# Kernel tuning notes

Hardware: AMD Instinct MI355X
Metric: run time of the kernel (lower is better)

Reference implementation:

```python
import jax, jax.numpy as jnp
import numpy as np

BS, SEQ, D_IN, D_OUT = 4, 1024, 1024, 1024
N_SKILLS, RANK = 8, 4
SCALING = 1.0  # lora_alpha / rank, folded into one constant
NEG_INF = -1e38


def setup_inputs() -> dict:
    key = jax.random.key(0)
    ks = jax.random.split(key, 5)
    x = jax.random.normal(ks[0], (BS, SEQ, D_IN), jnp.float32)
    phi = jax.random.normal(ks[1], (D_IN, N_SKILLS), jnp.float32) * 0.02
    lora_a = jax.random.normal(ks[2], (N_SKILLS, D_IN, RANK), jnp.float32) * 0.02
    lora_b = jax.random.normal(ks[3], (N_SKILLS, RANK, D_OUT), jnp.float32) * 0.02
    W = jax.random.normal(ks[4], (D_OUT, D_IN), jnp.float32) * 0.02
    b = jnp.zeros((D_OUT,), jnp.float32)
    # left-padded sequences with an instruction prefix right after the padding
    pad_len = np.array([100, 0, 250, 50])
    inst_len = 300
    pad = np.zeros((BS, SEQ), np.int32)
    inst = np.zeros((BS, SEQ), np.int32)
    for i in range(BS):
        pad[i, pad_len[i]:] = 1
        inst[i, pad_len[i]:pad_len[i] + inst_len] = 1
    return {"x": x, "phi": phi, "lora_a": lora_a, "lora_b": lora_b,
            "W": W, "b": b,
            "inst_mask": jnp.asarray(inst), "pad_mask": jnp.asarray(pad)}


def _causal_prefix_mask(inst_mask, pad_mask):
    # faithful port of create_causal_prefix_mask (padding_side='left')
    bs, seq = inst_mask.shape
    first_one = jnp.argmax(inst_mask, axis=1, keepdims=True)          # [b,1]
    n_ones = jnp.sum(inst_mask, axis=1, keepdims=True)                # [b,1]
    thresh = first_one + n_ones                                       # last_one_idx + 1
    exp = jnp.broadcast_to(thresh, (bs, seq))                         # [b,s]
    inv = jnp.maximum(seq - exp - jnp.arange(seq)[None, :], 0)[:, ::-1]
    m = (exp + inv) * pad_mask                                        # [b,s]
    m3 = m[:, :, None] * pad_mask[:, None, :]                         # [b,s,s]
    ar = jnp.arange(seq)[None, None, :]
    return ar < m3                                                    # bool [b,s,s]


def reference(x, phi, lora_a, lora_b, W, b, inst_mask, pad_mask):
    # router: mixing logits per token per skill
    mw = jnp.einsum('bsd,dn->bsn', x, phi)                            # [b,s,k]
    cm = _causal_prefix_mask(inst_mask, pad_mask)                     # [b,s,s]
    padf = pad_mask.astype(x.dtype)
    # expand over attended positions p, mask, softmax over p
    logits = jnp.where(cm[..., None], mw[:, :, None, :], NEG_INF)     # [b,s,p,k]
    logits = jnp.transpose(logits, (0, 3, 1, 2))                      # [b,k,s,p]
    D = jax.nn.softmax(logits, axis=-1)
    D = D * padf[:, None, :, None]                                    # zero padded query rows
    # token mixing: contract over source tokens (last axis of D)
    input_mixed = jnp.einsum('bsd,bkps->bkpd', x, D)                  # [b,k,s,d]
    # per-skill LoRA (n_splits == 1, q squeezed)
    ar_r = jnp.einsum('bksd,kdr->bskr', input_mixed, lora_a)          # [b,s,k,r]
    ad = jnp.einsum('bskr,krd->bskd', ar_r, lora_b)                   # [b,s,k,d_out]
    # softmax-weighted combine over skills
    C = jax.nn.softmax(mw, axis=-1)
    adapter_out = jnp.einsum('bsk,bskd->bsd', C, ad) * SCALING
    base = jnp.einsum('bsd,od->bso', x, W) + b
    return base + adapter_out
```

## Files before the change

### kernel.cpp

```cpp
#include <hip/hip_runtime.h>
#include <hip/hip_bf16.h>
#include <cstdint>

#define SEQ   1024
#define DOUT  1024
#define KDIM  1024
#define MTOT  4096

typedef __bf16 bf16x8 __attribute__((ext_vector_type(8)));
typedef float  f32x4  __attribute__((ext_vector_type(4)));
typedef unsigned short ushort8v __attribute__((ext_vector_type(8)));

__device__ inline unsigned short f2bf(float f) {
  union { float f; unsigned u; } a; a.f = f;
  unsigned r = a.u + 0x7fff + ((a.u >> 16) & 1);
  return (unsigned short)(r >> 16);
}

__device__ inline void gl16(const void* g, void* l) {
  __builtin_amdgcn_global_load_lds((__attribute__((address_space(1))) void*)g,
                                   (__attribute__((address_space(3))) void*)l, 16, 0, 0);
}

__device__ inline void barf() {
  asm volatile("" ::: "memory");
  __builtin_amdgcn_s_barrier();
  asm volatile("" ::: "memory");
}

__global__ __launch_bounds__(256) void k_prep(const float* __restrict__ phi, const float* __restrict__ la,
                                              const float* __restrict__ lb, const int* __restrict__ inst,
                                              unsigned short* __restrict__ Wc, unsigned short* __restrict__ B2T,
                                              int* __restrict__ thr) {
  int blk = blockIdx.x, tid = threadIdx.x;
  if (blk < 192) {
    int i = blk * 256 + tid;
    int row = 1024 + (i >> 10), d = i & 1023;
    float v;
    if (row < 1032)       v = phi[d * 8 + (row - 1024)];
    else if (row < 1064)  { int kr = row - 1032; v = la[(kr >> 2) * 4096 + d * 4 + (kr & 3)]; }
    else                  v = 0.f;
    Wc[(size_t)row * 1024 + d] = f2bf(v);
  } else if (blk < 320) {
    int i = (blk - 192) * 256 + tid;
    int n = i >> 5, kr = i & 31;
    B2T[i] = f2bf(lb[kr * 1024 + n]);
  } else {
    int b = tid >> 6, lane = tid & 63;
    int fo = 1 << 30, no = 0;
#pragma unroll
    for (int j = 0; j < 16; ++j) {
      int p = j * 64 + lane;
      int iv = inst[b * SEQ + p];
      if (iv > 0) fo = min(fo, p);
      no += iv;
    }
#pragma unroll
    for (int d = 1; d < 64; d <<= 1) { fo = min(fo, __shfl_xor(fo, d)); no += __shfl_xor(no, d); }
    if (lane == 0) thr[b] = (no > 0) ? fo + no : 0;
  }
}

__global__ __launch_bounds__(256) void k_mwz(const float* __restrict__ x,
                                             const float4* __restrict__ x4, ushort4* __restrict__ xb4,
                                             const unsigned short* __restrict__ Wc0,
                                             const float* __restrict__ W,
                                             unsigned short* __restrict__ Wc,
                                             float* __restrict__ mwzP) {
  __shared__ __align__(16) unsigned short As[64 * 32];
  __shared__ __align__(16) unsigned short Bs[48 * 32];
  int blk = blockIdx.x, t = threadIdx.x;
  if (blk >= 256) {
    if (blk < 4352) {
      size_t i = (size_t)(blk - 256) * 256 + t;
      float4 v = x4[i];
      ushort4 o; o.x = f2bf(v.x); o.y = f2bf(v.y); o.z = f2bf(v.z); o.w = f2bf(v.w);
      xb4[i] = o;
    } else {
      size_t i = (size_t)(blk - 4352) * 256 + t;
      Wc[i] = f2bf(W[i]);
    }
    return;
  }
  int bm = blk & 63, ks = blk >> 6;
  int wave = t >> 6, lane = t & 63;
  int quad = lane >> 4, lr = lane & 15;
  f32x4 acc[3];
#pragma unroll
  for (int i = 0; i < 3; ++i) acc[i] = (f32x4){0.f, 0.f, 0.f, 0.f};
  const float* aF = x + (size_t)(bm * 64) * KDIM + ks * 256;
  const unsigned short* bG = Wc0 + (size_t)1024 * KDIM + ks * 256;
  int r0 = t >> 2, c0 = (t & 3) * 8;
  const float* aP = aF + (size_t)r0 * KDIM + c0;
  float4 a0 = *(const float4*)(aP);
  float4 a1 = *(const float4*)(aP + 4);
  for (int kb = 0; kb < 256; kb += 32) {
    barf();
    ushort8v u;
    u[0] = f2bf(a0.x); u[1] = f2bf(a0.y); u[2] = f2bf(a0.z); u[3] = f2bf(a0.w);
    u[4] = f2bf(a1.x); u[5] = f2bf(a1.y); u[6] = f2bf(a1.z); u[7] = f2bf(a1.w);
    *reinterpret_cast<__shared__ ushort8v*>(&As[t * 8]) = u;
    if (t < 192) gl16(bG + (size_t)r0 * KDIM + kb + c0, &Bs[wave * 512]);
    if (kb + 32 < 256) {
      asm volatile("" ::: "memory");
      a0 = *(const float4*)(aP + kb + 32);
      a1 = *(const float4*)(aP + kb + 36);
      asm volatile("s_waitcnt vmcnt(2) lgkmcnt(0)" ::: "memory");
    } else {
      asm volatile("s_waitcnt vmcnt(0) lgkmcnt(0)" ::: "memory");
    }
    barf();
    bf16x8 af = *(const bf16x8*)&As[(wave * 16 + lr) * 32 + quad * 8];
#pragma unroll
    for (int ni = 0; ni < 3; ++ni) {
      bf16x8 bfr = *(const bf16x8*)&Bs[(ni * 16 + lr) * 32 + quad * 8];
      acc[ni] = __builtin_amdgcn_mfma_f32_16x16x32_bf16(af, bfr, acc[ni], 0, 0, 0);
    }
  }
#pragma unroll
  for (int ni = 0; ni < 3; ++ni) {
    int c = ni * 16 + lr;
#pragma unroll
    for (int rg = 0; rg < 4; ++rg) {
      int row = bm * 64 + wave * 16 + quad * 4 + rg;
      if (c < 40) mwzP[(size_t)(ks * 40 + c) * MTOT + row] = acc[ni][rg];
    }
  }
}

__global__ __launch_bounds__(1024) void k_scan_gate(const float* __restrict__ mwzP,
                                                    const int* __restrict__ pad, const int* __restrict__ thr,
                                                    unsigned short* __restrict__ gb) {
  int b = blockIdx.x, c = blockIdx.y;
  int tid = threadIdx.x, wv = tid >> 6, lane = tid & 63;
  __shared__ float wsz[16], wsp[16];
  __shared__ float sv, spc;
  int q = b * SEQ + tid;
  float pm = (float)pad[q];
  float z = 0.f;
#pragma unroll
  for (int s = 0; s < 4; ++s) z += mwzP[(size_t)(s * 40 + 8 + c) * MTOT + q];
  z *= pm;
  float vz = z, vp = pm;
#pragma unroll
  for (int d = 1; d < 64; d <<= 1) {
    float oz = __shfl_up(vz, d), op = __shfl_up(vp, d);
    if (lane >= d) { vz += oz; vp += op; }
  }
  if (lane == 63) { wsz[wv] = vz; wsp[wv] = vp; }
  __syncthreads();
  if (wv == 0 && lane < 16) {
    float oz = wsz[lane], op = wsp[lane], sz = oz, sp = op;
#pragma unroll
    for (int d = 1; d < 16; d <<= 1) {
      float tz = __shfl_up(sz, d), tp = __shfl_up(sp, d);
      if (lane >= d) { sz += tz; sp += tp; }
    }
    wsz[lane] = sz - oz; wsp[lane] = sp - op;
  }
  __syncthreads();
  vz += wsz[wv]; vp += wsp[wv];
  int th = thr[b];
  if (th > 0 && tid == th - 1) { sv = vz; spc = vp; }
  __syncthreads();
  unsigned short o = 0;
  if (pm != 0.f) {
    bool own = (tid + 1 >= th);
    float Tv  = own ? vz : sv;
    float cnt = own ? vp : spc;
    float C[8], mx = -1e30f;
#pragma unroll
    for (int k = 0; k < 8; ++k) {
      float m = 0.f;
#pragma unroll
      for (int s = 0; s < 4; ++s) m += mwzP[(size_t)(s * 40 + k) * MTOT + q];
      C[k] = m; mx = fmaxf(mx, m);
    }
    float sm = 0.f;
#pragma unroll
    for (int k = 0; k < 8; ++k) { C[k] = __expf(C[k] - mx); sm += C[k]; }
    o = f2bf(C[c >> 2] * Tv / (sm * cnt));
  }
  gb[(size_t)q * 32 + c] = o;
}

__global__ __launch_bounds__(256) void k_gemm(const unsigned short* __restrict__ A,
                                              const unsigned short* __restrict__ Wc,
                                              const unsigned short* __restrict__ gb,
                                              const unsigned short* __restrict__ B2T,
                                              float* __restrict__ out,
                                              const float* __restrict__ bias) {
  __shared__ __align__(16) unsigned short As[2][128 * 64];
  __shared__ __align__(16) unsigned short Bs[2][64 * 64];
  int bm = blockIdx.x, bn = blockIdx.y;
  int t = threadIdx.x;
  int wave = t >> 6, lane = t & 63;
  int wr = wave >> 1, wc = wave & 1;
  int quad = lane >> 4, lr = lane & 15;
  f32x4 acc[4][2];
#pragma unroll
  for (int i = 0; i < 4; i++)
#pragma unroll
    for (int j = 0; j < 2; j++) acc[i][j] = (f32x4){0.f, 0.f, 0.f, 0.f};

  {
    bf16x8 ga[4], gBf[2];
#pragma unroll
    for (int mi = 0; mi < 4; mi++)
      ga[mi] = *(const bf16x8*)(gb + (size_t)(bm * 128 + wr * 64 + mi * 16 + lr) * 32 + quad * 8);
#pragma unroll
    for (int ni = 0; ni < 2; ni++)
      gBf[ni] = *(const bf16x8*)(B2T + (size_t)(bn * 64 + wc * 32 + ni * 16 + lr) * 32 + quad * 8);
#pragma unroll
    for (int mi = 0; mi < 4; mi++)
#pragma unroll
      for (int ni = 0; ni < 2; ni++)
        acc[mi][ni] = __builtin_amdgcn_mfma_f32_16x16x32_bf16(ga[mi], gBf[ni], acc[mi][ni], 0, 0, 0);
  }

  const unsigned short* aG = A + (size_t)bm * 128 * KDIM;
  const unsigned short* bG = Wc + (size_t)bn * 64 * KDIM;

  auto stage = [&](int b, int kb) {
#pragma unroll
    for (int i = 0; i < 4; ++i) {
      int g = i * 256 + t;
      int r = g >> 3, c = (g & 7) * 8;
      int cs = c ^ ((r & 7) * 8);
      gl16(aG + (size_t)r * KDIM + kb + cs, &As[b][i * 2048 + wave * 512]);
    }
#pragma unroll
    for (int i = 0; i < 2; ++i) {
      int g = i * 256 + t;
      int r = g >> 3, c = (g & 7) * 8;
      int cs = c ^ ((r & 7) * 8);
      gl16(bG + (size_t)r * KDIM + kb + cs, &Bs[b][i * 2048 + wave * 512]);
    }
  };

  stage(0, 0);
  asm volatile("s_waitcnt vmcnt(0)" ::: "memory");
  barf();
  for (int it = 0; it < 16; ++it) {
    int cur = it & 1;
    if (it < 15) {
      stage(cur ^ 1, (it + 1) * 64);
      asm volatile("s_waitcnt vmcnt(6)" ::: "memory");
    } else {
      asm volatile("s_waitcnt vmcnt(0)" ::: "memory");
    }
    barf();
#pragma unroll
    for (int kk = 0; kk < 2; ++kk) {
      bf16x8 af[4], bfr[2];
#pragma unroll
      for (int mi = 0; mi < 4; mi++) {
        int R = wr * 64 + mi * 16 + lr;
        int cc = (kk * 32 + quad * 8) ^ ((R & 7) * 8);
        af[mi] = *(const bf16x8*)&As[cur][R * 64 + cc];
      }
#pragma unroll
      for (int ni = 0; ni < 2; ni++) {
        int R = wc * 32 + ni * 16 + lr;
        int cc = (kk * 32 + quad * 8) ^ ((R & 7) * 8);
        bfr[ni] = *(const bf16x8*)&Bs[cur][R * 64 + cc];
      }
#pragma unroll
      for (int mi = 0; mi < 4; mi++)
#pragma unroll
        for (int ni = 0; ni < 2; ni++)
          acc[mi][ni] = __builtin_amdgcn_mfma_f32_16x16x32_bf16(af[mi], bfr[ni], acc[mi][ni], 0, 0, 0);
    }
    barf();
  }

#pragma unroll
  for (int mi = 0; mi < 4; mi++) {
#pragma unroll
    for (int ni = 0; ni < 2; ni++) {
      int col = bn * 64 + wc * 32 + ni * 16 + lr;
      float bv = bias[col];
#pragma unroll
      for (int rg = 0; rg < 4; ++rg) {
        int row = bm * 128 + wr * 64 + mi * 16 + quad * 4 + rg;
        out[(size_t)row * DOUT + col] = acc[mi][ni][rg] + bv;
      }
    }
  }
}

extern "C" void kernel_launch(void* const* d_in, const int* in_sizes, int n_in,
                              void* d_out, int out_size, void* d_ws, size_t ws_size,
                              hipStream_t stream) {
  const float* x    = (const float*)d_in[0];
  const float* phi  = (const float*)d_in[1];
  const float* la   = (const float*)d_in[2];
  const float* lb   = (const float*)d_in[3];
  const float* W    = (const float*)d_in[4];
  const float* bias = (const float*)d_in[5];
  const int*   inst = (const int*)d_in[6];
  const int*   pad  = (const int*)d_in[7];
  float* out = (float*)d_out;

  char* ws = (char*)d_ws;
  unsigned short* xb  = (unsigned short*)ws;
  unsigned short* Wc  = (unsigned short*)(ws + 8388608);
  unsigned short* B2T = (unsigned short*)(ws + 10584064);
  float* mwzP = (float*)(ws + 10649600);
  unsigned short* gb  = (unsigned short*)(ws + 13271040);
  int*   thr  = (int*)(ws + 13533184);

  hipLaunchKernelGGL(k_prep,      dim3(321),    dim3(256),  0, stream,
                     phi, la, lb, inst, Wc, B2T, thr);
  hipLaunchKernelGGL(k_mwz,       dim3(8448),   dim3(256),  0, stream,
                     x, (const float4*)x, (ushort4*)xb, Wc, W, Wc, mwzP);
  hipLaunchKernelGGL(k_scan_gate, dim3(4, 32),  dim3(1024), 0, stream, mwzP, pad, thr, gb);
  hipLaunchKernelGGL(k_gemm,      dim3(32, 16), dim3(256),  0, stream, xb, Wc, gb, B2T, out, bias);
}
```

Before: 111.1 us.

## Merge prep into router kernel and use two-wave 128x64 GEMM tiles

Removes the separate prep launch by folding phi/lora_a/lora_b conversion and threshold computation into the front kernel. The router blocks now load their 256-wide K slice of x into registers once and build the bf16 phi/lora_a B tile directly in swizzled shared memory, instead of looping with staged loads. The main GEMM drops to 128 threads, with each wave computing 64x64 instead of 64x32, which doubles per-wave operand reuse but halves waves per block and may reduce latency hiding. Router blocks now redundantly convert phi/la from strided fp32 reads, 64 times per K slice.

```diff
diff --git a/kernel.cpp b/kernel.cpp
--- a/kernel.cpp
+++ b/kernel.cpp
@@ -28,47 +28,14 @@
   asm volatile("" ::: "memory");
 }
 
-__global__ __launch_bounds__(256) void k_prep(const float* __restrict__ phi, const float* __restrict__ la,
-                                              const float* __restrict__ lb, const int* __restrict__ inst,
-                                              unsigned short* __restrict__ Wc, unsigned short* __restrict__ B2T,
-                                              int* __restrict__ thr) {
-  int blk = blockIdx.x, tid = threadIdx.x;
-  if (blk < 192) {
-    int i = blk * 256 + tid;
-    int row = 1024 + (i >> 10), d = i & 1023;
-    float v;
-    if (row < 1032)       v = phi[d * 8 + (row - 1024)];
-    else if (row < 1064)  { int kr = row - 1032; v = la[(kr >> 2) * 4096 + d * 4 + (kr & 3)]; }
-    else                  v = 0.f;
-    Wc[(size_t)row * 1024 + d] = f2bf(v);
-  } else if (blk < 320) {
-    int i = (blk - 192) * 256 + tid;
-    int n = i >> 5, kr = i & 31;
-    B2T[i] = f2bf(lb[kr * 1024 + n]);
-  } else {
-    int b = tid >> 6, lane = tid & 63;
-    int fo = 1 << 30, no = 0;
-#pragma unroll
-    for (int j = 0; j < 16; ++j) {
-      int p = j * 64 + lane;
-      int iv = inst[b * SEQ + p];
-      if (iv > 0) fo = min(fo, p);
-      no += iv;
-    }
-#pragma unroll
-    for (int d = 1; d < 64; d <<= 1) { fo = min(fo, __shfl_xor(fo, d)); no += __shfl_xor(no, d); }
-    if (lane == 0) thr[b] = (no > 0) ? fo + no : 0;
-  }
-}
-
-__global__ __launch_bounds__(256) void k_mwz(const float* __restrict__ x,
-                                             const float4* __restrict__ x4, ushort4* __restrict__ xb4,
-                                             const unsigned short* __restrict__ Wc0,
-                                             const float* __restrict__ W,
-                                             unsigned short* __restrict__ Wc,
-                                             float* __restrict__ mwzP) {
-  __shared__ __align__(16) unsigned short As[64 * 32];
-  __shared__ __align__(16) unsigned short Bs[48 * 32];
+__global__ __launch_bounds__(256) void k_front(const float* __restrict__ x,
+                                               const float4* __restrict__ x4, ushort4* __restrict__ xb4,
+                                               const float* __restrict__ phi, const float* __restrict__ la,
+                                               const float* __restrict__ lb, const float* __restrict__ W,
+                                               const int* __restrict__ inst,
+                                               unsigned short* __restrict__ Wc, unsigned short* __restrict__ B2T,
+                                               int* __restrict__ thr, float* __restrict__ mwzP) {
+  __shared__ __align__(16) unsigned short Bs8[8 * 48 * 32];
   int blk = blockIdx.x, t = threadIdx.x;
   if (blk >= 256) {
     if (blk < 4352) {
@@ -76,45 +43,85 @@
       float4 v = x4[i];
       ushort4 o; o.x = f2bf(v.x); o.y = f2bf(v.y); o.z = f2bf(v.z); o.w = f2bf(v.w);
       xb4[i] = o;
-    } else {
+    } else if (blk < 8448) {
       size_t i = (size_t)(blk - 4352) * 256 + t;
       Wc[i] = f2bf(W[i]);
+    } else if (blk < 8576) {
+      int i = (blk - 8448) * 256 + t;
+      int n = i >> 5, kr = i & 31;
+      B2T[i] = f2bf(lb[kr * 1024 + n]);
+    } else {
+      int b = t >> 6, lane = t & 63;
+      int fo = 1 << 30, no = 0;
+#pragma unroll
+      for (int j = 0; j < 16; ++j) {
+        int p = j * 64 + lane;
+        int iv = inst[b * SEQ + p];
+        if (iv > 0) fo = min(fo, p);
+        no += iv;
+      }
+#pragma unroll
+      for (int d = 1; d < 64; d <<= 1) { fo = min(fo, __shfl_xor(fo, d)); no += __shfl_xor(no, d); }
+      if (lane == 0) thr[b] = (no > 0) ? fo + no : 0;
     }
     return;
   }
   int bm = blk & 63, ks = blk >> 6;
   int wave = t >> 6, lane = t & 63;
   int quad = lane >> 4, lr = lane & 15;
+  bf16x8 af[8];
+  {
+    const float* aP = x + (size_t)(bm * 64 + wave * 16 + lr) * KDIM + ks * 256 + quad * 8;
+#pragma unroll
+    for (int s = 0; s < 8; ++s) {
+      float4 u0 = *(const float4*)(aP + s * 32);
+      float4 u1 = *(const float4*)(aP + s * 32 + 4);
+      bf16x8 v;
+      v[0] = (__bf16)u0.x; v[1] = (__bf16)u0.y; v[2] = (__bf16)u0.z; v[3] = (__bf16)u0.w;
+      v[4] = (__bf16)u1.x; v[5] = (__bf16)u1.y; v[6] = (__bf16)u1.z; v[7] = (__bf16)u1.w;
+      af[s] = v;
+    }
+  }
+  if (t < 192) {
+    int rb = t >> 2, c0 = (t & 3) * 8;
+    int sw = (rb & 3) * 8;
+    const float4* la4 = (const float4*)la;
+#pragma unroll
+    for (int s = 0; s < 8; ++s) {
+      ushort8v u;
+      if (rb < 8) {
+#pragma unroll
+        for (int j = 0; j < 8; ++j) {
+          int d = ks * 256 + s * 32 + c0 + j;
+          u[j] = f2bf(phi[d * 8 + rb]);
+        }
+      } else if (rb < 40) {
+        int kr = rb - 8;
+#pragma unroll
+        for (int j = 0; j < 8; ++j) {
+          int d = ks * 256 + s * 32 + c0 + j;
+          float4 v = la4[(size_t)(kr >> 2) * 1024 + d];
+          float vv = (kr & 3) == 0 ? v.x : (kr & 3) == 1 ? v.y : (kr & 3) == 2 ? v.z : v.w;
+          u[j] = f2bf(vv);
+        }
+      } else {
+#pragma unroll
+        for (int j = 0; j < 8; ++j) u[j] = 0;
+      }
+      *reinterpret_cast<__shared__ ushort8v*>(&Bs8[s * 1536 + rb * 32 + (c0 ^ sw)]) = u;
+    }
+  }
+  __syncthreads();
   f32x4 acc[3];
 #pragma unroll
   for (int i = 0; i < 3; ++i) acc[i] = (f32x4){0.f, 0.f, 0.f, 0.f};
-  const float* aF = x + (size_t)(bm * 64) * KDIM + ks * 256;
-  const unsigned short* bG = Wc0 + (size_t)1024 * KDIM + ks * 256;
-  int r0 = t >> 2, c0 = (t & 3) * 8;
-  const float* aP = aF + (size_t)r0 * KDIM + c0;
-  float4 a0 = *(const float4*)(aP);
-  float4 a1 = *(const float4*)(aP + 4);
-  for (int kb = 0; kb < 256; kb += 32) {
-    barf();
-    ushort8v u;
-    u[0] = f2bf(a0.x); u[1] = f2bf(a0.y); u[2] = f2bf(a0.z); u[3] = f2bf(a0.w);
-    u[4] = f2bf(a1.x); u[5] = f2bf(a1.y); u[6] = f2bf(a1.z); u[7] = f2bf(a1.w);
-    *reinterpret_cast<__shared__ ushort8v*>(&As[t * 8]) = u;
-    if (t < 192) gl16(bG + (size_t)r0 * KDIM + kb + c0, &Bs[wave * 512]);
-    if (kb + 32 < 256) {
-      asm volatile("" ::: "memory");
-      a0 = *(const float4*)(aP + kb + 32);
-      a1 = *(const float4*)(aP + kb + 36);
-      asm volatile("s_waitcnt vmcnt(2) lgkmcnt(0)" ::: "memory");
-    } else {
-      asm volatile("s_waitcnt vmcnt(0) lgkmcnt(0)" ::: "memory");
-    }
-    barf();
-    bf16x8 af = *(const bf16x8*)&As[(wave * 16 + lr) * 32 + quad * 8];
+#pragma unroll
+  for (int s = 0; s < 8; ++s) {
 #pragma unroll
     for (int ni = 0; ni < 3; ++ni) {
-      bf16x8 bfr = *(const bf16x8*)&Bs[(ni * 16 + lr) * 32 + quad * 8];
-      acc[ni] = __builtin_amdgcn_mfma_f32_16x16x32_bf16(af, bfr, acc[ni], 0, 0, 0);
+      int rB = ni * 16 + lr;
+      bf16x8 bfr = *(const bf16x8*)&Bs8[s * 1536 + rB * 32 + ((quad * 8) ^ ((rB & 3) * 8))];
+      acc[ni] = __builtin_amdgcn_mfma_f32_16x16x32_bf16(af[s], bfr, acc[ni], 0, 0, 0);
     }
   }
 #pragma unroll
@@ -184,7 +191,7 @@
   gb[(size_t)q * 32 + c] = o;
 }
 
-__global__ __launch_bounds__(256) void k_gemm(const unsigned short* __restrict__ A,
+__global__ __launch_bounds__(128) void k_gemm(const unsigned short* __restrict__ A,
                                               const unsigned short* __restrict__ Wc,
                                               const unsigned short* __restrict__ gb,
                                               const unsigned short* __restrict__ B2T,
@@ -195,26 +202,25 @@
   int bm = blockIdx.x, bn = blockIdx.y;
   int t = threadIdx.x;
   int wave = t >> 6, lane = t & 63;
-  int wr = wave >> 1, wc = wave & 1;
   int quad = lane >> 4, lr = lane & 15;
-  f32x4 acc[4][2];
+  f32x4 acc[4][4];
 #pragma unroll
   for (int i = 0; i < 4; i++)
 #pragma unroll
-    for (int j = 0; j < 2; j++) acc[i][j] = (f32x4){0.f, 0.f, 0.f, 0.f};
+    for (int j = 0; j < 4; j++) acc[i][j] = (f32x4){0.f, 0.f, 0.f, 0.f};
 
   {
-    bf16x8 ga[4], gBf[2];
+    bf16x8 ga[4], gBf[4];
 #pragma unroll
     for (int mi = 0; mi < 4; mi++)
-      ga[mi] = *(const bf16x8*)(gb + (size_t)(bm * 128 + wr * 64 + mi * 16 + lr) * 32 + quad * 8);
-#pragma unroll
-    for (int ni = 0; ni < 2; ni++)
-      gBf[ni] = *(const bf16x8*)(B2T + (size_t)(bn * 64 + wc * 32 + ni * 16 + lr) * 32 + quad * 8);
+      ga[mi] = *(const bf16x8*)(gb + (size_t)(bm * 128 + wave * 64 + mi * 16 + lr) * 32 + quad * 8);
+#pragma unroll
+    for (int ni = 0; ni < 4; ni++)
+      gBf[ni] = *(const bf16x8*)(B2T + (size_t)(bn * 64 + ni * 16 + lr) * 32 + quad * 8);
 #pragma unroll
     for (int mi = 0; mi < 4; mi++)
 #pragma unroll
-      for (int ni = 0; ni < 2; ni++)
+      for (int ni = 0; ni < 4; ni++)
         acc[mi][ni] = __builtin_amdgcn_mfma_f32_16x16x32_bf16(ga[mi], gBf[ni], acc[mi][ni], 0, 0, 0);
   }
 
@@ -223,18 +229,18 @@
 
   auto stage = [&](int b, int kb) {
 #pragma unroll
-    for (int i = 0; i < 4; ++i) {
-      int g = i * 256 + t;
+    for (int i = 0; i < 8; ++i) {
+      int g = i * 128 + t;
       int r = g >> 3, c = (g & 7) * 8;
       int cs = c ^ ((r & 7) * 8);
-      gl16(aG + (size_t)r * KDIM + kb + cs, &As[b][i * 2048 + wave * 512]);
-    }
-#pragma unroll
-    for (int i = 0; i < 2; ++i) {
-      int g = i * 256 + t;
+      gl16(aG + (size_t)r * KDIM + kb + cs, &As[b][i * 1024 + wave * 512]);
+    }
+#pragma unroll
+    for (int i = 0; i < 4; ++i) {
+      int g = i * 128 + t;
       int r = g >> 3, c = (g & 7) * 8;
       int cs = c ^ ((r & 7) * 8);
-      gl16(bG + (size_t)r * KDIM + kb + cs, &Bs[b][i * 2048 + wave * 512]);
+      gl16(bG + (size_t)r * KDIM + kb + cs, &Bs[b][i * 1024 + wave * 512]);
     }
   };
 
@@ -245,30 +251,30 @@
     int cur = it & 1;
     if (it < 15) {
       stage(cur ^ 1, (it + 1) * 64);
-      asm volatile("s_waitcnt vmcnt(6)" ::: "memory");
+      asm volatile("s_waitcnt vmcnt(12)" ::: "memory");
     } else {
       asm volatile("s_waitcnt vmcnt(0)" ::: "memory");
     }
     barf();
 #pragma unroll
     for (int kk = 0; kk < 2; ++kk) {
-      bf16x8 af[4], bfr[2];
+      bf16x8 af[4], bfr[4];
 #pragma unroll
       for (int mi = 0; mi < 4; mi++) {
-        int R = wr * 64 + mi * 16 + lr;
+        int R = wave * 64 + mi * 16 + lr;
         int cc = (kk * 32 + quad * 8) ^ ((R & 7) * 8);
         af[mi] = *(const bf16x8*)&As[cur][R * 64 + cc];
       }
 #pragma unroll
-      for (int ni = 0; ni < 2; ni++) {
-        int R = wc * 32 + ni * 16 + lr;
+      for (int ni = 0; ni < 4; ni++) {
+        int R = ni * 16 + lr;
         int cc = (kk * 32 + quad * 8) ^ ((R & 7) * 8);
         bfr[ni] = *(const bf16x8*)&Bs[cur][R * 64 + cc];
       }
 #pragma unroll
       for (int mi = 0; mi < 4; mi++)
 #pragma unroll
-        for (int ni = 0; ni < 2; ni++)
+        for (int ni = 0; ni < 4; ni++)
           acc[mi][ni] = __builtin_amdgcn_mfma_f32_16x16x32_bf16(af[mi], bfr[ni], acc[mi][ni], 0, 0, 0);
     }
     barf();
@@ -277,12 +283,12 @@
 #pragma unroll
   for (int mi = 0; mi < 4; mi++) {
 #pragma unroll
-    for (int ni = 0; ni < 2; ni++) {
-      int col = bn * 64 + wc * 32 + ni * 16 + lr;
+    for (int ni = 0; ni < 4; ni++) {
+      int col = bn * 64 + ni * 16 + lr;
       float bv = bias[col];
 #pragma unroll
       for (int rg = 0; rg < 4; ++rg) {
-        int row = bm * 128 + wr * 64 + mi * 16 + quad * 4 + rg;
+        int row = bm * 128 + wave * 64 + mi * 16 + quad * 4 + rg;
         out[(size_t)row * DOUT + col] = acc[mi][ni][rg] + bv;
       }
     }
@@ -310,10 +316,9 @@
   unsigned short* gb  = (unsigned short*)(ws + 13271040);
   int*   thr  = (int*)(ws + 13533184);
 
-  hipLaunchKernelGGL(k_prep,      dim3(321),    dim3(256),  0, stream,
-                     phi, la, lb, inst, Wc, B2T, thr);
-  hipLaunchKernelGGL(k_mwz,       dim3(8448),   dim3(256),  0, stream,
-                     x, (const float4*)x, (ushort4*)xb, Wc, W, Wc, mwzP);
+  hipLaunchKernelGGL(k_front,     dim3(8577),   dim3(256),  0, stream,
+                     x, (const float4*)x, (ushort4*)xb, phi, la, lb, W, inst,
+                     Wc, B2T, thr, mwzP);
   hipLaunchKernelGGL(k_scan_gate, dim3(4, 32),  dim3(1024), 0, stream, mwzP, pad, thr, gb);
-  hipLaunchKernelGGL(k_gemm,      dim3(32, 16), dim3(256),  0, stream, xb, Wc, gb, B2T, out, bias);
-}
+  hipLaunchKernelGGL(k_gemm,      dim3(32, 16), dim3(128),  0, stream, xb, Wc, gb, B2T, out, bias);
+}
```

Measured after the change: 122.3 us. 1.1x slower.
